# Optimization experiments

Hardware: AMD Instinct MI355X
Metric: run time of the kernel (lower is better)

Reference implementation:

```python
import jax, jax.numpy as jnp
import numpy as np

B, NI, NO = 32, 64, 64


def setup_inputs() -> dict:
    key = jax.random.key(0)
    k1, k2, k3, k4, k5, k6 = jax.random.split(key, 6)
    return {
        "input_re": jax.random.normal(k1, (B, NI, NI), dtype=jnp.float32),
        "input_im": jax.random.normal(k2, (B, NI, NI), dtype=jnp.float32),
        "w_re": jax.random.normal(k3, (NI, NI, NO, NO), dtype=jnp.float32),
        "w_im": jax.random.normal(k4, (NI, NI, NO, NO), dtype=jnp.float32),
        "amp_weights": jax.random.normal(k5, (NI, NI), dtype=jnp.float32),
        "phase_weights": jax.random.normal(k6, (NI, NI), dtype=jnp.float32),
    }


def reference(input_re, input_im, w_re, w_im, amp_weights, phase_weights):
    # complex input field (B, NI, NI) and diffraction kernel (NI, NI, NO, NO)
    e_in = jax.lax.complex(input_re, input_im)
    w_ip = jax.lax.complex(w_re, w_im)
    # passive transmission coefficients: sigmoid(amp) * exp(i*phase)
    ts = (jax.nn.sigmoid(amp_weights)
          * jnp.exp(1j * phase_weights.astype(jnp.complex64))).astype(jnp.complex64)
    # modulated field, then sum over input pixels (i,j) -> complex GEMM
    modulated = e_in * ts[None, :, :]                    # (B, NI, NI)
    out = jnp.einsum('bij,ijkl->bkl', modulated, w_ip)   # (B, NO, NO)
    return out
```

## Files before the change

### kernel.cpp

```cpp
#include <hip/hip_runtime.h>
#include <cstdint>
#include <cstddef>

#define KC 4096
#define NN 4096
#define NB 32
#define HALF (NB * NN)
#define KB 32

typedef __attribute__((ext_vector_type(8))) short  bf16x8;
typedef __attribute__((ext_vector_type(16))) float f32x16;

__device__ __forceinline__ unsigned short f2bf(float f) {
    union { float f; unsigned u; } v; v.f = f;
    unsigned r = v.u + 0x7fffu + ((v.u >> 16) & 1u);
    return (unsigned short)(r >> 16);
}

__global__ __launch_bounds__(256) void prep_kernel(
    const float* __restrict__ in_re, const float* __restrict__ in_im,
    const float* __restrict__ amp,   const float* __restrict__ phase,
    uint32_t* __restrict__ wsA)
{
    int tid = blockIdx.x * 256 + threadIdx.x;
    int b = tid >> 12;
    int k = tid & (KC - 1);
    float er = in_re[tid], ei = in_im[tid];
    float a = amp[k], p = phase[k];
    float s = 1.0f / (1.0f + __expf(-a));
    float sn = __sinf(p);
    float cs = __cosf(p);
    float tr = s * cs, ti = s * sn;
    float mr = er * tr - ei * ti;
    float mi = er * ti + ei * tr;
    uint32_t pk = (uint32_t)f2bf(mr) | ((uint32_t)f2bf(mi) << 16);
    wsA[((((k >> 2) << 5) + b) << 2) | (k & 3)] = pk;
}

__global__ __launch_bounds__(512) void gemm_kernel(
    const float* __restrict__ w_re, const float* __restrict__ w_im,
    const uint32_t* __restrict__ wsA, float2* __restrict__ wsP, int steps)
{
    __shared__ float    ldsW[2][2][KB][256];
    __shared__ uint32_t ldsA[2][KB * 32];

    const int tid  = threadIdx.x;
    const int lane = tid & 63;
    const int wave = tid >> 6;
    const int h    = lane >> 5;
    const int l32  = lane & 31;
    const int n    = blockIdx.x * 256 + wave * 32 + l32;
    const int s    = blockIdx.y;
    const int kbase = s * (steps * KB);

    const float* gW_re = w_re + (size_t)kbase * NN + blockIdx.x * 256 + (lane << 2);
    const float* gW_im = w_im + (size_t)kbase * NN + blockIdx.x * 256 + (lane << 2);
    const uint32_t* gA = wsA + (size_t)(kbase >> 2) * 128 + lane;

    f32x16 accR = {};
    f32x16 accI = {};

    auto STAGE = [&](int t, int bb) {
#pragma unroll
        for (int j = 0; j < 4; ++j) {
            int row = j * 8 + wave;
            __builtin_amdgcn_global_load_lds(
                (const __attribute__((address_space(1))) void*)(gW_re + (size_t)(t * KB + row) * NN),
                (__attribute__((address_space(3))) void*)(&ldsW[bb][0][row][0]),
                16, 0, 0);
        }
#pragma unroll
        for (int j = 0; j < 4; ++j) {
            int row = j * 8 + wave;
            __builtin_amdgcn_global_load_lds(
                (const __attribute__((address_space(1))) void*)(gW_im + (size_t)(t * KB + row) * NN),
                (__attribute__((address_space(3))) void*)(&ldsW[bb][1][row][0]),
                16, 0, 0);
        }
#pragma unroll
        for (int j = 0; j < 2; ++j) {
            int c = wave * 2 + j;
            __builtin_amdgcn_global_load_lds(
                (const __attribute__((address_space(1))) void*)(gA + (size_t)t * (KB * 32) + c * 64),
                (__attribute__((address_space(3))) void*)(&ldsA[bb][c * 64]),
                4, 0, 0);
        }
    };

    auto COMPUTE = [&](int bb) {
#pragma unroll
        for (int ss = 0; ss < 4; ++ss) {
            bf16x8 afrag = *(const bf16x8*)&ldsA[bb][ss * 256 + h * 128 + l32 * 4];
            const float* Lre = &ldsW[bb][0][ss * 8 + h * 4][wave * 32 + l32];
            const float* Lim = &ldsW[bb][1][ss * 8 + h * 4][wave * 32 + l32];
            float r0 = Lre[0], r1 = Lre[256], r2 = Lre[512], r3 = Lre[768];
            float i0 = Lim[0], i1 = Lim[256], i2 = Lim[512], i3 = Lim[768];

            unsigned short br0 = f2bf(r0), br1 = f2bf(r1), br2 = f2bf(r2), br3 = f2bf(r3);
            unsigned short bi0 = f2bf(i0), bi1 = f2bf(i1), bi2 = f2bf(i2), bi3 = f2bf(i3);
            bf16x8 bR, bI;
            bR[0] = (short)br0;  bR[1] = (short)(bi0 ^ 0x8000);
            bR[2] = (short)br1;  bR[3] = (short)(bi1 ^ 0x8000);
            bR[4] = (short)br2;  bR[5] = (short)(bi2 ^ 0x8000);
            bR[6] = (short)br3;  bR[7] = (short)(bi3 ^ 0x8000);
            bI[0] = (short)bi0;  bI[1] = (short)br0;
            bI[2] = (short)bi1;  bI[3] = (short)br1;
            bI[4] = (short)bi2;  bI[5] = (short)br2;
            bI[6] = (short)bi3;  bI[7] = (short)br3;

            accR = __builtin_amdgcn_mfma_f32_32x32x16_bf16(afrag, bR, accR, 0, 0, 0);
            accI = __builtin_amdgcn_mfma_f32_32x32x16_bf16(afrag, bI, accI, 0, 0, 0);
        }
    };

    STAGE(0, 0);
    for (int t = 0; t < steps - 1; ++t) {
        STAGE(t + 1, (t + 1) & 1);
        asm volatile("s_waitcnt vmcnt(10)" ::: "memory");
        __builtin_amdgcn_s_barrier();
        COMPUTE(t & 1);
        __builtin_amdgcn_s_barrier();
    }
    asm volatile("s_waitcnt vmcnt(0)" ::: "memory");
    __builtin_amdgcn_s_barrier();
    COMPUTE((steps - 1) & 1);

#pragma unroll
    for (int r = 0; r < 16; ++r) {
        int brow = (r & 3) + 8 * (r >> 2) + 4 * h;
        float2 v; v.x = accR[r]; v.y = accI[r];
        wsP[((size_t)s * NB + brow) * NN + n] = v;
    }
}

__global__ __launch_bounds__(256) void reduce_kernel(
    const float4* __restrict__ wsP, float* __restrict__ out, int S)
{
    int tid = blockIdx.x * 256 + threadIdx.x;
    float re0 = 0.f, im0 = 0.f, re1 = 0.f, im1 = 0.f;
#pragma unroll 8
    for (int s = 0; s < S; ++s) {
        float4 v = wsP[(size_t)s * (NB * NN / 2) + tid];
        re0 += v.x; im0 += v.y; re1 += v.z; im1 += v.w;
    }
    float2* o_re = (float2*)out + tid;
    float2* o_im = (float2*)(out + HALF) + tid;
    *o_re = make_float2(re0, re1);
    *o_im = make_float2(im0, im1);
}

extern "C" void kernel_launch(void* const* d_in, const int* in_sizes, int n_in,
                              void* d_out, int out_size, void* d_ws, size_t ws_size,
                              hipStream_t stream)
{
    const float* in_re  = (const float*)d_in[0];
    const float* in_im  = (const float*)d_in[1];
    const float* w_re   = (const float*)d_in[2];
    const float* w_im   = (const float*)d_in[3];
    const float* amp    = (const float*)d_in[4];
    const float* phase  = (const float*)d_in[5];

    const size_t A_BYTES = (size_t)1024 * 32 * 16;
    uint32_t* wsA = (uint32_t*)d_ws;
    float2*   wsP = (float2*)((char*)d_ws + A_BYTES);

    int S = 16;
    while (S > 1 && A_BYTES + (size_t)S * NB * NN * sizeof(float2) > ws_size) S >>= 1;
    int steps = (KC / S) / KB;

    prep_kernel<<<dim3((NB * KC) / 256), dim3(256), 0, stream>>>(
        in_re, in_im, amp, phase, wsA);

    gemm_kernel<<<dim3(NN / 256, S), dim3(512), 0, stream>>>(
        w_re, w_im, wsA, wsP, steps);

    reduce_kernel<<<dim3((NB * NN / 2) / 256), dim3(256), 0, stream>>>(
        (const float4*)wsP, (float*)d_out, S);
}
```

Baseline: 164.0 us.

## Fuse prep, GEMM and reduction into one cooperative kernel with grid syncs

Replaces the three separate launches (prep, split-K GEMM, reduce) with a single cooperative kernel. Grid-wide syncs separate the phases, and prep and reduce use grid-stride loops. This removes two kernel launch gaps and their inter-kernel dependency bubbles. In exchange it adds two grid barriers and runs the prep and reduce phases on only 256 blocks of 512 threads, which may lower their parallelism. The old three-kernel path remains as a fallback if the cooperative launch fails.

```diff
diff --git a/kernel.cpp b/kernel.cpp
--- a/kernel.cpp
+++ b/kernel.cpp
@@ -1,4 +1,5 @@
 #include <hip/hip_runtime.h>
+#include <hip/hip_cooperative_groups.h>
 #include <cstdint>
 #include <cstddef>
 
@@ -17,15 +18,14 @@
     return (unsigned short)(r >> 16);
 }
 
-__global__ __launch_bounds__(256) void prep_kernel(
-    const float* __restrict__ in_re, const float* __restrict__ in_im,
-    const float* __restrict__ amp,   const float* __restrict__ phase,
+__device__ __forceinline__ void prep_body(
+    int gtid, const float* __restrict__ in_re, const float* __restrict__ in_im,
+    const float* __restrict__ amp, const float* __restrict__ phase,
     uint32_t* __restrict__ wsA)
 {
-    int tid = blockIdx.x * 256 + threadIdx.x;
-    int b = tid >> 12;
-    int k = tid & (KC - 1);
-    float er = in_re[tid], ei = in_im[tid];
+    int b = gtid >> 12;
+    int k = gtid & (KC - 1);
+    float er = in_re[gtid], ei = in_im[gtid];
     float a = amp[k], p = phase[k];
     float s = 1.0f / (1.0f + __expf(-a));
     float sn = __sinf(p);
@@ -35,6 +35,142 @@
     float mi = er * ti + ei * tr;
     uint32_t pk = (uint32_t)f2bf(mr) | ((uint32_t)f2bf(mi) << 16);
     wsA[((((k >> 2) << 5) + b) << 2) | (k & 3)] = pk;
+}
+
+__global__ __launch_bounds__(512) void fused_kernel(
+    const float* __restrict__ in_re, const float* __restrict__ in_im,
+    const float* __restrict__ amp,   const float* __restrict__ phase,
+    const float* __restrict__ w_re,  const float* __restrict__ w_im,
+    uint32_t* __restrict__ wsA, float2* __restrict__ wsP,
+    float* __restrict__ out, int S, int steps)
+{
+    cooperative_groups::grid_group grid = cooperative_groups::this_grid();
+
+    __shared__ float    ldsW[2][2][KB][256];
+    __shared__ uint32_t ldsA[2][KB * 32];
+
+    const int tid    = threadIdx.x;
+    const int nblk   = gridDim.x;
+    const int gthr   = nblk * 512;
+
+    for (int g = blockIdx.x * 512 + tid; g < NB * KC; g += gthr)
+        prep_body(g, in_re, in_im, amp, phase, wsA);
+
+    grid.sync();
+
+    {
+        const int bidx = blockIdx.x & 15;
+        const int s    = blockIdx.x >> 4;
+        const int lane = tid & 63;
+        const int wave = tid >> 6;
+        const int h    = lane >> 5;
+        const int l32  = lane & 31;
+        const int n    = bidx * 256 + wave * 32 + l32;
+        const int kbase = s * (steps * KB);
+
+        const float* gW_re = w_re + (size_t)kbase * NN + bidx * 256 + (lane << 2);
+        const float* gW_im = w_im + (size_t)kbase * NN + bidx * 256 + (lane << 2);
+        const uint32_t* gA = wsA + (size_t)(kbase >> 2) * 128 + lane;
+
+        f32x16 accR = {};
+        f32x16 accI = {};
+
+        auto STAGE = [&](int t, int bb) {
+#pragma unroll
+            for (int j = 0; j < 4; ++j) {
+                int row = j * 8 + wave;
+                __builtin_amdgcn_global_load_lds(
+                    (const __attribute__((address_space(1))) void*)(gW_re + (size_t)(t * KB + row) * NN),
+                    (__attribute__((address_space(3))) void*)(&ldsW[bb][0][row][0]),
+                    16, 0, 0);
+            }
+#pragma unroll
+            for (int j = 0; j < 4; ++j) {
+                int row = j * 8 + wave;
+                __builtin_amdgcn_global_load_lds(
+                    (const __attribute__((address_space(1))) void*)(gW_im + (size_t)(t * KB + row) * NN),
+                    (__attribute__((address_space(3))) void*)(&ldsW[bb][1][row][0]),
+                    16, 0, 0);
+            }
+#pragma unroll
+            for (int j = 0; j < 2; ++j) {
+                int c = wave * 2 + j;
+                __builtin_amdgcn_global_load_lds(
+                    (const __attribute__((address_space(1))) void*)(gA + (size_t)t * (KB * 32) + c * 64),
+                    (__attribute__((address_space(3))) void*)(&ldsA[bb][c * 64]),
+                    4, 0, 0);
+            }
+        };
+
+        auto COMPUTE = [&](int bb) {
+#pragma unroll
+            for (int ss = 0; ss < 4; ++ss) {
+                bf16x8 afrag = *(const bf16x8*)&ldsA[bb][ss * 256 + h * 128 + l32 * 4];
+                const float* Lre = &ldsW[bb][0][ss * 8 + h * 4][wave * 32 + l32];
+                const float* Lim = &ldsW[bb][1][ss * 8 + h * 4][wave * 32 + l32];
+                float r0 = Lre[0], r1 = Lre[256], r2 = Lre[512], r3 = Lre[768];
+                float i0 = Lim[0], i1 = Lim[256], i2 = Lim[512], i3 = Lim[768];
+
+                unsigned short br0 = f2bf(r0), br1 = f2bf(r1), br2 = f2bf(r2), br3 = f2bf(r3);
+                unsigned short bi0 = f2bf(i0), bi1 = f2bf(i1), bi2 = f2bf(i2), bi3 = f2bf(i3);
+                bf16x8 bR, bI;
+                bR[0] = (short)br0;  bR[1] = (short)(bi0 ^ 0x8000);
+                bR[2] = (short)br1;  bR[3] = (short)(bi1 ^ 0x8000);
+                bR[4] = (short)br2;  bR[5] = (short)(bi2 ^ 0x8000);
+                bR[6] = (short)br3;  bR[7] = (short)(bi3 ^ 0x8000);
+                bI[0] = (short)bi0;  bI[1] = (short)br0;
+                bI[2] = (short)bi1;  bI[3] = (short)br1;
+                bI[4] = (short)bi2;  bI[5] = (short)br2;
+                bI[6] = (short)bi3;  bI[7] = (short)br3;
+
+                accR = __builtin_amdgcn_mfma_f32_32x32x16_bf16(afrag, bR, accR, 0, 0, 0);
+                accI = __builtin_amdgcn_mfma_f32_32x32x16_bf16(afrag, bI, accI, 0, 0, 0);
+            }
+        };
+
+        STAGE(0, 0);
+        for (int t = 0; t < steps - 1; ++t) {
+            STAGE(t + 1, (t + 1) & 1);
+            asm volatile("s_waitcnt vmcnt(10)" ::: "memory");
+            __builtin_amdgcn_s_barrier();
+            COMPUTE(t & 1);
+            __builtin_amdgcn_s_barrier();
+        }
+        asm volatile("s_waitcnt vmcnt(0)" ::: "memory");
+        __builtin_amdgcn_s_barrier();
+        COMPUTE((steps - 1) & 1);
+
+#pragma unroll
+        for (int r = 0; r < 16; ++r) {
+            int brow = (r & 3) + 8 * (r >> 2) + 4 * h;
+            float2 v; v.x = accR[r]; v.y = accI[r];
+            wsP[((size_t)s * NB + brow) * NN + n] = v;
+        }
+    }
+
+    grid.sync();
+
+    {
+        const float4* wsP4 = (const float4*)wsP;
+        for (int t = blockIdx.x * 512 + tid; t < NB * NN / 2; t += gthr) {
+            float re0 = 0.f, im0 = 0.f, re1 = 0.f, im1 = 0.f;
+            for (int s = 0; s < S; ++s) {
+                float4 v = wsP4[(size_t)s * (NB * NN / 2) + t];
+                re0 += v.x; im0 += v.y; re1 += v.z; im1 += v.w;
+            }
+            ((float2*)out)[t]          = make_float2(re0, re1);
+            ((float2*)(out + HALF))[t] = make_float2(im0, im1);
+        }
+    }
+}
+
+__global__ __launch_bounds__(256) void prep_kernel(
+    const float* __restrict__ in_re, const float* __restrict__ in_im,
+    const float* __restrict__ amp,   const float* __restrict__ phase,
+    uint32_t* __restrict__ wsA)
+{
+    int tid = blockIdx.x * 256 + threadIdx.x;
+    prep_body(tid, in_re, in_im, amp, phase, wsA);
 }
 
 __global__ __launch_bounds__(512) void gemm_kernel(
@@ -163,17 +299,26 @@
     const size_t A_BYTES = (size_t)1024 * 32 * 16;
     uint32_t* wsA = (uint32_t*)d_ws;
     float2*   wsP = (float2*)((char*)d_ws + A_BYTES);
+    float*    outp = (float*)d_out;
 
     int S = 16;
     while (S > 1 && A_BYTES + (size_t)S * NB * NN * sizeof(float2) > ws_size) S >>= 1;
     int steps = (KC / S) / KB;
 
-    prep_kernel<<<dim3((NB * KC) / 256), dim3(256), 0, stream>>>(
-        in_re, in_im, amp, phase, wsA);
-
-    gemm_kernel<<<dim3(NN / 256, S), dim3(512), 0, stream>>>(
-        w_re, w_im, wsA, wsP, steps);
-
-    reduce_kernel<<<dim3((NB * NN / 2) / 256), dim3(256), 0, stream>>>(
-        (const float4*)wsP, (float*)d_out, S);
-}
+    void* args[] = {
+        (void*)&in_re, (void*)&in_im, (void*)&amp, (void*)&phase,
+        (void*)&w_re, (void*)&w_im,
+        (void*)&wsA, (void*)&wsP, (void*)&outp, (void*)&S, (void*)&steps
+    };
+    hipError_t err = hipLaunchCooperativeKernel(
+        (const void*)fused_kernel, dim3(16 * S), dim3(512), args, 0, stream);
+
+    if (err != hipSuccess) {
+        prep_kernel<<<dim3((NB * KC) / 256), dim3(256), 0, stream>>>(
+            in_re, in_im, amp, phase, wsA);
+        gemm_kernel<<<dim3(NN / 256, S), dim3(512), 0, stream>>>(
+            w_re, w_im, wsA, wsP, steps);
+        reduce_kernel<<<dim3((NB * NN / 2) / 256), dim3(256), 0, stream>>>(
+            (const float4*)wsP, outp, S);
+    }
+}
```

After: 242.1 us. 1.48x slower.

## Templatize GEMM split-K and widen N tile with S=32 split

Applied to the files above, without the earlier changes.

The GEMM kernel becomes a template over the split-K factor. The S=32 variant uses a 512-column N tile with two accumulator groups per wave and a 16-row K block, and runs 8x32 blocks with launch bounds allowing two blocks per CU. This is meant to reuse each A fragment across more columns and to raise occupancy and parallelism when streaming the large weight tensor. In exchange it writes twice as many partial results for the reduce kernel to sum, which adds workspace traffic.

```diff
diff --git a/kernel.cpp b/kernel.cpp
--- a/kernel.cpp
+++ b/kernel.cpp
@@ -6,7 +6,6 @@
 #define NN 4096
 #define NB 32
 #define HALF (NB * NN)
-#define KB 32
 
 typedef __attribute__((ext_vector_type(8))) short  bf16x8;
 typedef __attribute__((ext_vector_type(16))) float f32x16;
@@ -37,51 +36,60 @@
     wsA[((((k >> 2) << 5) + b) << 2) | (k & 3)] = pk;
 }
 
-__global__ __launch_bounds__(512) void gemm_kernel(
+template <int S_>
+__global__ __launch_bounds__(512, 2) void gemm_tmpl(
     const float* __restrict__ w_re, const float* __restrict__ w_im,
-    const uint32_t* __restrict__ wsA, float2* __restrict__ wsP, int steps)
-{
-    __shared__ float    ldsW[2][2][KB][256];
-    __shared__ uint32_t ldsA[2][KB * 32];
+    const uint32_t* __restrict__ wsA, float2* __restrict__ wsP)
+{
+    constexpr int KBk  = 512 / S_;
+    constexpr int NT   = 16 * S_;
+    constexpr int CG   = NT / 256;
+    constexpr int CHR  = NT / 256;
+    constexpr int PR   = 2 * KBk;
+    constexpr int PRW  = PR / 8;
+    constexpr int AGW  = KBk / 16;
+    constexpr int SS   = KBk / 8;
+    constexpr int STEPS = (KC / S_) / KBk;
+
+    __shared__ float    ldsW[2][2][KBk][NT];
+    __shared__ uint32_t ldsA[2][KBk * 32];
 
     const int tid  = threadIdx.x;
     const int lane = tid & 63;
     const int wave = tid >> 6;
     const int h    = lane >> 5;
     const int l32  = lane & 31;
-    const int n    = blockIdx.x * 256 + wave * 32 + l32;
+    const int bidx = blockIdx.x;
     const int s    = blockIdx.y;
-    const int kbase = s * (steps * KB);
-
-    const float* gW_re = w_re + (size_t)kbase * NN + blockIdx.x * 256 + (lane << 2);
-    const float* gW_im = w_im + (size_t)kbase * NN + blockIdx.x * 256 + (lane << 2);
+    const int kbase = s * (KC / S_);
+
     const uint32_t* gA = wsA + (size_t)(kbase >> 2) * 128 + lane;
 
-    f32x16 accR = {};
-    f32x16 accI = {};
+    f32x16 accR[CG] = {};
+    f32x16 accI[CG] = {};
 
     auto STAGE = [&](int t, int bb) {
 #pragma unroll
-        for (int j = 0; j < 4; ++j) {
-            int row = j * 8 + wave;
+        for (int i = 0; i < PRW; ++i) {
+            int pr    = wave * PRW + i;
+            int plane = pr / KBk;
+            int row   = pr % KBk;
+            const float* wp = plane ? w_im : w_re;
+            const float* gsrc = wp + (size_t)(kbase + t * KBk + row) * NN
+                                   + bidx * NT + (lane << 2);
+#pragma unroll
+            for (int c = 0; c < CHR; ++c) {
+                __builtin_amdgcn_global_load_lds(
+                    (const __attribute__((address_space(1))) void*)(gsrc + c * 256),
+                    (__attribute__((address_space(3))) void*)(&ldsW[bb][plane][row][c * 256]),
+                    16, 0, 0);
+            }
+        }
+#pragma unroll
+        for (int j = 0; j < AGW; ++j) {
+            int c = wave * AGW + j;
             __builtin_amdgcn_global_load_lds(
-                (const __attribute__((address_space(1))) void*)(gW_re + (size_t)(t * KB + row) * NN),
-                (__attribute__((address_space(3))) void*)(&ldsW[bb][0][row][0]),
-                16, 0, 0);
-        }
-#pragma unroll
-        for (int j = 0; j < 4; ++j) {
-            int row = j * 8 + wave;
-            __builtin_amdgcn_global_load_lds(
-                (const __attribute__((address_space(1))) void*)(gW_im + (size_t)(t * KB + row) * NN),
-                (__attribute__((address_space(3))) void*)(&ldsW[bb][1][row][0]),
-                16, 0, 0);
-        }
-#pragma unroll
-        for (int j = 0; j < 2; ++j) {
-            int c = wave * 2 + j;
-            __builtin_amdgcn_global_load_lds(
-                (const __attribute__((address_space(1))) void*)(gA + (size_t)t * (KB * 32) + c * 64),
+                (const __attribute__((address_space(1))) void*)(gA + (size_t)t * (KBk * 32) + c * 64),
                 (__attribute__((address_space(3))) void*)(&ldsA[bb][c * 64]),
                 4, 0, 0);
         }
@@ -89,47 +97,58 @@
 
     auto COMPUTE = [&](int bb) {
 #pragma unroll
-        for (int ss = 0; ss < 4; ++ss) {
+        for (int ss = 0; ss < SS; ++ss) {
             bf16x8 afrag = *(const bf16x8*)&ldsA[bb][ss * 256 + h * 128 + l32 * 4];
-            const float* Lre = &ldsW[bb][0][ss * 8 + h * 4][wave * 32 + l32];
-            const float* Lim = &ldsW[bb][1][ss * 8 + h * 4][wave * 32 + l32];
-            float r0 = Lre[0], r1 = Lre[256], r2 = Lre[512], r3 = Lre[768];
-            float i0 = Lim[0], i1 = Lim[256], i2 = Lim[512], i3 = Lim[768];
-
-            unsigned short br0 = f2bf(r0), br1 = f2bf(r1), br2 = f2bf(r2), br3 = f2bf(r3);
-            unsigned short bi0 = f2bf(i0), bi1 = f2bf(i1), bi2 = f2bf(i2), bi3 = f2bf(i3);
-            bf16x8 bR, bI;
-            bR[0] = (short)br0;  bR[1] = (short)(bi0 ^ 0x8000);
-            bR[2] = (short)br1;  bR[3] = (short)(bi1 ^ 0x8000);
-            bR[4] = (short)br2;  bR[5] = (short)(bi2 ^ 0x8000);
-            bR[6] = (short)br3;  bR[7] = (short)(bi3 ^ 0x8000);
-            bI[0] = (short)bi0;  bI[1] = (short)br0;
-            bI[2] = (short)bi1;  bI[3] = (short)br1;
-            bI[4] = (short)bi2;  bI[5] = (short)br2;
-            bI[6] = (short)bi3;  bI[7] = (short)br3;
-
-            accR = __builtin_amdgcn_mfma_f32_32x32x16_bf16(afrag, bR, accR, 0, 0, 0);
-            accI = __builtin_amdgcn_mfma_f32_32x32x16_bf16(afrag, bI, accI, 0, 0, 0);
+#pragma unroll
+            for (int cg = 0; cg < CG; ++cg) {
+                const int col = cg * 256 + wave * 32 + l32;
+                const float* Lre = &ldsW[bb][0][ss * 8 + h * 4][col];
+                const float* Lim = &ldsW[bb][1][ss * 8 + h * 4][col];
+                float r0 = Lre[0], r1 = Lre[NT], r2 = Lre[2 * NT], r3 = Lre[3 * NT];
+                float i0 = Lim[0], i1 = Lim[NT], i2 = Lim[2 * NT], i3 = Lim[3 * NT];
+
+                unsigned short br0 = f2bf(r0), br1 = f2bf(r1), br2 = f2bf(r2), br3 = f2bf(r3);
+                unsigned short bi0 = f2bf(i0), bi1 = f2bf(i1), bi2 = f2bf(i2), bi3 = f2bf(i3);
+                bf16x8 bR, bI;
+                bR[0] = (short)br0;  bR[1] = (short)(bi0 ^ 0x8000);
+                bR[2] = (short)br1;  bR[3] = (short)(bi1 ^ 0x8000);
+                bR[4] = (short)br2;  bR[5] = (short)(bi2 ^ 0x8000);
+                bR[6] = (short)br3;  bR[7] = (short)(bi3 ^ 0x8000);
+                bI[0] = (short)bi0;  bI[1] = (short)br0;
+                bI[2] = (short)bi1;  bI[3] = (short)br1;
+                bI[4] = (short)bi2;  bI[5] = (short)br2;
+                bI[6] = (short)bi3;  bI[7] = (short)br3;
+
+                accR[cg] = __builtin_amdgcn_mfma_f32_32x32x16_bf16(afrag, bR, accR[cg], 0, 0, 0);
+                accI[cg] = __builtin_amdgcn_mfma_f32_32x32x16_bf16(afrag, bI, accI[cg], 0, 0, 0);
+            }
         }
     };
 
     STAGE(0, 0);
-    for (int t = 0; t < steps - 1; ++t) {
+    for (int t = 0; t < STEPS - 1; ++t) {
         STAGE(t + 1, (t + 1) & 1);
-        asm volatile("s_waitcnt vmcnt(10)" ::: "memory");
+        if constexpr (S_ == 32)
+            asm volatile("s_waitcnt vmcnt(9)" ::: "memory");
+        else
+            asm volatile("s_waitcnt vmcnt(10)" ::: "memory");
         __builtin_amdgcn_s_barrier();
         COMPUTE(t & 1);
         __builtin_amdgcn_s_barrier();
     }
     asm volatile("s_waitcnt vmcnt(0)" ::: "memory");
     __builtin_amdgcn_s_barrier();
-    COMPUTE((steps - 1) & 1);
-
-#pragma unroll
-    for (int r = 0; r < 16; ++r) {
-        int brow = (r & 3) + 8 * (r >> 2) + 4 * h;
-        float2 v; v.x = accR[r]; v.y = accI[r];
-        wsP[((size_t)s * NB + brow) * NN + n] = v;
+    COMPUTE((STEPS - 1) & 1);
+
+#pragma unroll
+    for (int cg = 0; cg < CG; ++cg) {
+        const int n = bidx * NT + cg * 256 + wave * 32 + l32;
+#pragma unroll
+        for (int r = 0; r < 16; ++r) {
+            int brow = (r & 3) + 8 * (r >> 2) + 4 * h;
+            float2 v; v.x = accR[cg][r]; v.y = accI[cg][r];
+            wsP[((size_t)s * NB + brow) * NN + n] = v;
+        }
     }
 }
 
@@ -164,15 +183,19 @@
     uint32_t* wsA = (uint32_t*)d_ws;
     float2*   wsP = (float2*)((char*)d_ws + A_BYTES);
 
-    int S = 16;
-    while (S > 1 && A_BYTES + (size_t)S * NB * NN * sizeof(float2) > ws_size) S >>= 1;
-    int steps = (KC / S) / KB;
+    int S = 32;
+    if (A_BYTES + (size_t)32 * NB * NN * sizeof(float2) > ws_size) S = 16;
 
     prep_kernel<<<dim3((NB * KC) / 256), dim3(256), 0, stream>>>(
         in_re, in_im, amp, phase, wsA);
 
-    gemm_kernel<<<dim3(NN / 256, S), dim3(512), 0, stream>>>(
-        w_re, w_im, wsA, wsP, steps);
+    if (S == 32) {
+        gemm_tmpl<32><<<dim3(NN / 512, 32), dim3(512), 0, stream>>>(
+            w_re, w_im, wsA, wsP);
+    } else {
+        gemm_tmpl<16><<<dim3(NN / 256, 16), dim3(512), 0, stream>>>(
+            w_re, w_im, wsA, wsP);
+    }
 
     reduce_kernel<<<dim3((NB * NN / 2) / 256), dim3(256), 0, stream>>>(
         (const float4*)wsP, (float*)d_out, S);
```

Measured after the change: 171.1 us. 4.3% more time.

## Fuse modulation prep into split-K GEMM, preload A slice into LDS

Applied to the files above, without the earlier changes.

Removes the separate prep kernel. Each GEMM block now computes its own 256-wide K slice of modulated bf16 inputs directly into LDS once, before the main loop. The W tile depth is halved to 16 rows per stage, and the split count is hardcoded to 16 with an occupancy hint of two blocks per CU. This drops one launch plus the workspace round trip for A, but every N-block recomputes the same A slice. The split count is also fixed, so it no longer shrinks when the workspace is small.

```diff
diff --git a/kernel.cpp b/kernel.cpp
--- a/kernel.cpp
+++ b/kernel.cpp
@@ -6,7 +6,10 @@
 #define NN 4096
 #define NB 32
 #define HALF (NB * NN)
-#define KB 32
+#define S_SPLIT 16
+#define KBk 16
+#define NT 256
+#define STEPS ((KC / S_SPLIT) / KBk)
 
 typedef __attribute__((ext_vector_type(8))) short  bf16x8;
 typedef __attribute__((ext_vector_type(16))) float f32x16;
@@ -17,84 +20,73 @@
     return (unsigned short)(r >> 16);
 }
 
-__global__ __launch_bounds__(256) void prep_kernel(
+__global__ __launch_bounds__(512, 2) void fused_gemm(
     const float* __restrict__ in_re, const float* __restrict__ in_im,
     const float* __restrict__ amp,   const float* __restrict__ phase,
-    uint32_t* __restrict__ wsA)
+    const float* __restrict__ w_re,  const float* __restrict__ w_im,
+    float2* __restrict__ wsP)
 {
-    int tid = blockIdx.x * 256 + threadIdx.x;
-    int b = tid >> 12;
-    int k = tid & (KC - 1);
-    float er = in_re[tid], ei = in_im[tid];
-    float a = amp[k], p = phase[k];
-    float s = 1.0f / (1.0f + __expf(-a));
-    float sn = __sinf(p);
-    float cs = __cosf(p);
-    float tr = s * cs, ti = s * sn;
-    float mr = er * tr - ei * ti;
-    float mi = er * ti + ei * tr;
-    uint32_t pk = (uint32_t)f2bf(mr) | ((uint32_t)f2bf(mi) << 16);
-    wsA[((((k >> 2) << 5) + b) << 2) | (k & 3)] = pk;
-}
-
-__global__ __launch_bounds__(512) void gemm_kernel(
-    const float* __restrict__ w_re, const float* __restrict__ w_im,
-    const uint32_t* __restrict__ wsA, float2* __restrict__ wsP, int steps)
-{
-    __shared__ float    ldsW[2][2][KB][256];
-    __shared__ uint32_t ldsA[2][KB * 32];
+    __shared__ float    ldsW[2][2][KBk][NT];
+    __shared__ uint32_t ldsA[8192];
 
     const int tid  = threadIdx.x;
     const int lane = tid & 63;
     const int wave = tid >> 6;
     const int h    = lane >> 5;
     const int l32  = lane & 31;
-    const int n    = blockIdx.x * 256 + wave * 32 + l32;
+    const int bidx = blockIdx.x;
     const int s    = blockIdx.y;
-    const int kbase = s * (steps * KB);
+    const int kbase = s * (KC / S_SPLIT);
 
-    const float* gW_re = w_re + (size_t)kbase * NN + blockIdx.x * 256 + (lane << 2);
-    const float* gW_im = w_im + (size_t)kbase * NN + blockIdx.x * 256 + (lane << 2);
-    const uint32_t* gA = wsA + (size_t)(kbase >> 2) * 128 + lane;
+    {
+        const int k_local = tid & 255;
+        const int b0      = (tid >> 8) * 16;
+        const int kg      = kbase + k_local;
+        float a = amp[kg], p = phase[kg];
+        float sg = 1.0f / (1.0f + __expf(-a));
+        float sn = __sinf(p), cs = __cosf(p);
+        float tr = sg * cs, ti = sg * sn;
+#pragma unroll 4
+        for (int b = b0; b < b0 + 16; ++b) {
+            float er = in_re[b * KC + kg], ei = in_im[b * KC + kg];
+            float mr = er * tr - ei * ti;
+            float mi = er * ti + ei * tr;
+            ldsA[((k_local >> 2) * 32 + b) * 4 + (k_local & 3)] =
+                (uint32_t)f2bf(mr) | ((uint32_t)f2bf(mi) << 16);
+        }
+    }
+    __syncthreads();
+
+    const float* gW[2] = {
+        w_re + (size_t)kbase * NN + bidx * NT + (lane << 2),
+        w_im + (size_t)kbase * NN + bidx * NT + (lane << 2) };
 
     f32x16 accR = {};
     f32x16 accI = {};
 
     auto STAGE = [&](int t, int bb) {
 #pragma unroll
-        for (int j = 0; j < 4; ++j) {
-            int row = j * 8 + wave;
+        for (int i = 0; i < 4; ++i) {
+            int pr    = wave * 4 + i;
+            int plane = pr >> 4;
+            int row   = pr & 15;
             __builtin_amdgcn_global_load_lds(
-                (const __attribute__((address_space(1))) void*)(gW_re + (size_t)(t * KB + row) * NN),
-                (__attribute__((address_space(3))) void*)(&ldsW[bb][0][row][0]),
+                (const __attribute__((address_space(1))) void*)
+                    (gW[plane] + (size_t)(t * KBk + row) * NN),
+                (__attribute__((address_space(3))) void*)(&ldsW[bb][plane][row][0]),
                 16, 0, 0);
-        }
-#pragma unroll
-        for (int j = 0; j < 4; ++j) {
-            int row = j * 8 + wave;
-            __builtin_amdgcn_global_load_lds(
-                (const __attribute__((address_space(1))) void*)(gW_im + (size_t)(t * KB + row) * NN),
-                (__attribute__((address_space(3))) void*)(&ldsW[bb][1][row][0]),
-                16, 0, 0);
-        }
-#pragma unroll
-        for (int j = 0; j < 2; ++j) {
-            int c = wave * 2 + j;
-            __builtin_amdgcn_global_load_lds(
-                (const __attribute__((address_space(1))) void*)(gA + (size_t)t * (KB * 32) + c * 64),
-                (__attribute__((address_space(3))) void*)(&ldsA[bb][c * 64]),
-                4, 0, 0);
         }
     };
 
-    auto COMPUTE = [&](int bb) {
+    auto COMPUTE = [&](int t, int bb) {
 #pragma unroll
-        for (int ss = 0; ss < 4; ++ss) {
-            bf16x8 afrag = *(const bf16x8*)&ldsA[bb][ss * 256 + h * 128 + l32 * 4];
+        for (int ss = 0; ss < 2; ++ss) {
+            const int o_s = t * 4 + ss * 2 + h;
+            bf16x8 afrag = *(const bf16x8*)&ldsA[(o_s * 32 + l32) * 4];
             const float* Lre = &ldsW[bb][0][ss * 8 + h * 4][wave * 32 + l32];
             const float* Lim = &ldsW[bb][1][ss * 8 + h * 4][wave * 32 + l32];
-            float r0 = Lre[0], r1 = Lre[256], r2 = Lre[512], r3 = Lre[768];
-            float i0 = Lim[0], i1 = Lim[256], i2 = Lim[512], i3 = Lim[768];
+            float r0 = Lre[0], r1 = Lre[NT], r2 = Lre[2 * NT], r3 = Lre[3 * NT];
+            float i0 = Lim[0], i1 = Lim[NT], i2 = Lim[2 * NT], i3 = Lim[3 * NT];
 
             unsigned short br0 = f2bf(r0), br1 = f2bf(r1), br2 = f2bf(r2), br3 = f2bf(r3);
             unsigned short bi0 = f2bf(i0), bi1 = f2bf(i1), bi2 = f2bf(i2), bi3 = f2bf(i3);
@@ -114,32 +106,35 @@
     };
 
     STAGE(0, 0);
-    for (int t = 0; t < steps - 1; ++t) {
+    for (int t = 0; t < STEPS - 1; ++t) {
         STAGE(t + 1, (t + 1) & 1);
-        asm volatile("s_waitcnt vmcnt(10)" ::: "memory");
+        asm volatile("s_waitcnt vmcnt(4)" ::: "memory");
         __builtin_amdgcn_s_barrier();
-        COMPUTE(t & 1);
+        COMPUTE(t, t & 1);
         __builtin_amdgcn_s_barrier();
     }
     asm volatile("s_waitcnt vmcnt(0)" ::: "memory");
     __builtin_amdgcn_s_barrier();
-    COMPUTE((steps - 1) & 1);
+    COMPUTE(STEPS - 1, (STEPS - 1) & 1);
 
+    {
+        const int n = bidx * NT + wave * 32 + l32;
 #pragma unroll
-    for (int r = 0; r < 16; ++r) {
-        int brow = (r & 3) + 8 * (r >> 2) + 4 * h;
-        float2 v; v.x = accR[r]; v.y = accI[r];
-        wsP[((size_t)s * NB + brow) * NN + n] = v;
+        for (int r = 0; r < 16; ++r) {
+            int brow = (r & 3) + 8 * (r >> 2) + 4 * h;
+            float2 v; v.x = accR[r]; v.y = accI[r];
+            wsP[((size_t)s * NB + brow) * NN + n] = v;
+        }
     }
 }
 
 __global__ __launch_bounds__(256) void reduce_kernel(
-    const float4* __restrict__ wsP, float* __restrict__ out, int S)
+    const float4* __restrict__ wsP, float* __restrict__ out)
 {
     int tid = blockIdx.x * 256 + threadIdx.x;
     float re0 = 0.f, im0 = 0.f, re1 = 0.f, im1 = 0.f;
 #pragma unroll 8
-    for (int s = 0; s < S; ++s) {
+    for (int s = 0; s < S_SPLIT; ++s) {
         float4 v = wsP[(size_t)s * (NB * NN / 2) + tid];
         re0 += v.x; im0 += v.y; re1 += v.z; im1 += v.w;
     }
@@ -160,20 +155,11 @@
     const float* amp    = (const float*)d_in[4];
     const float* phase  = (const float*)d_in[5];
 
-    const size_t A_BYTES = (size_t)1024 * 32 * 16;
-    uint32_t* wsA = (uint32_t*)d_ws;
-    float2*   wsP = (float2*)((char*)d_ws + A_BYTES);
+    float2* wsP = (float2*)d_ws;
 
-    int S = 16;
-    while (S > 1 && A_BYTES + (size_t)S * NB * NN * sizeof(float2) > ws_size) S >>= 1;
-    int steps = (KC / S) / KB;
-
-    prep_kernel<<<dim3((NB * KC) / 256), dim3(256), 0, stream>>>(
-        in_re, in_im, amp, phase, wsA);
-
-    gemm_kernel<<<dim3(NN / 256, S), dim3(512), 0, stream>>>(
-        w_re, w_im, wsA, wsP, steps);
+    fused_gemm<<<dim3(NN / NT, S_SPLIT), dim3(512), 0, stream>>>(
+        in_re, in_im, amp, phase, w_re, w_im, wsP);
 
     reduce_kernel<<<dim3((NB * NN / 2) / 256), dim3(256), 0, stream>>>(
-        (const float4*)wsP, (float*)d_out, S);
+        (const float4*)wsP, (float*)d_out);
 }
```

Result: no change. 164.5 us (+0.3%).
